# Optimization experiments

Measured on AMD Instinct MI355X. Metric: run time of the kernel, lower is better.

The kernel has to match this reference:

```python
import jax, jax.numpy as jnp
import numpy as np

GAMMA = 1.0

def setup_inputs() -> dict:
    key = jax.random.key(0)
    kx, ky = jax.random.split(key)
    x = jax.random.normal(kx, (8192, 256), dtype=jnp.float32)
    y = jax.random.normal(ky, (8192, 256), dtype=jnp.float32)
    return {"x": x, "y": y}

def reference(x, y):
    # RBF kernel K[i,j] = exp(-gamma * ||x_i - y_j||^2)
    # materializing the O(N*M*D) broadcast difference tensor.
    x2 = jnp.sum(x * x, axis=-1)            # [N]
    y2 = jnp.sum(y * y, axis=-1)            # [M]
    xy = jnp.einsum('nd,md->nm', x, y)      # [N, M] GEMM
    dist2 = x2[:, None] + y2[None, :] - 2.0 * xy
    dist2 = jnp.maximum(dist2, 0.0)         # guard tiny negative round-off
    return jnp.exp(-GAMMA * dist2)
```

## Files before the change

### kernel.cpp

```cpp
#include <hip/hip_runtime.h>


#define M_DIM 8192
#define K_DIM 256
#define BM 64
#define BN 64
#define TRS 68

typedef long frag8;
typedef __attribute__((ext_vector_type(4))) float float4v;

__global__ __launch_bounds__(256) void prep_kernel(
        const float* __restrict__ x, const float* __restrict__ y,
        unsigned char* __restrict__ xb, unsigned char* __restrict__ yb,
        float* __restrict__ x2, float* __restrict__ y2) {
    int row  = blockIdx.x * 4 + (threadIdx.x >> 6);
    int lane = threadIdx.x & 63;

    const float* src; unsigned char* dst; float* nrm; int r;
    if (row < M_DIM) { src = x; dst = xb; nrm = x2; r = row; }
    else             { src = y; dst = yb; nrm = y2; r = row - M_DIM; }

    const float4* s4 = (const float4*)(src + (size_t)r * K_DIM);
    float4 v = s4[lane];
    float ss = v.x * v.x + v.y * v.y + v.z * v.z + v.w * v.w;

    int packed = __builtin_amdgcn_cvt_pk_fp8_f32(v.x, v.y, 0, false);
    packed     = __builtin_amdgcn_cvt_pk_fp8_f32(v.z, v.w, packed, true);

    int u  = lane >> 2;
    int su = u ^ (r & 15);
    *(unsigned int*)(dst + (size_t)r * 256 + su * 16 + (lane & 3) * 4) =
        (unsigned int)packed;

    #pragma unroll
    for (int o = 32; o > 0; o >>= 1) ss += __shfl_down(ss, o);
    if (lane == 0) nrm[r] = ss;
}

__global__ __launch_bounds__(256, 4) void rbf_gemm(
        const unsigned char* __restrict__ xb, const unsigned char* __restrict__ yb,
        const float* __restrict__ x2, const float* __restrict__ y2,
        float* __restrict__ out) {
    __shared__ __align__(16) unsigned char smem[BM * 256 + BN * 256];
    unsigned char* As = smem;
    unsigned char* Bs = smem + BM * 256;
    float* T = (float*)smem;

    const int tid  = threadIdx.x;
    const int wid  = tid >> 6;
    const int lane = tid & 63;
    const int wm   = wid >> 1;
    const int wn   = wid & 1;

    const int bid = blockIdx.x;
    const int xcd = bid & 7;
    const int lin = bid >> 3;
    const int ty  = (xcd << 4) + (lin >> 7);
    const int tx  = lin & 127;
    const int m0  = ty * BM;
    const int n0  = tx * BN;

    #pragma unroll
    for (int i = 0; i < 4; ++i) {
        const int ch = wid * 4 + i;
        __builtin_amdgcn_global_load_lds(
            (__attribute__((address_space(1))) void*)
                (xb + (size_t)(m0 + ch * 4) * 256 + lane * 16),
            (__attribute__((address_space(3))) void*)&As[ch * 1024],
            16, 0, 0);
    }
    #pragma unroll
    for (int i = 0; i < 4; ++i) {
        const int ch = wid * 4 + i;
        __builtin_amdgcn_global_load_lds(
            (__attribute__((address_space(1))) void*)
                (yb + (size_t)(n0 + ch * 4) * 256 + lane * 16),
            (__attribute__((address_space(3))) void*)&Bs[ch * 1024],
            16, 0, 0);
    }

    const int q = lane >> 4;
    const int c = lane & 15;
    float x2v[2][4];
    float y2v[2];
    #pragma unroll
    for (int mt = 0; mt < 2; ++mt)
        #pragma unroll
        for (int v = 0; v < 4; ++v)
            x2v[mt][v] = x2[m0 + wm * 32 + mt * 16 + q * 4 + v];
    #pragma unroll
    for (int nt = 0; nt < 2; ++nt)
        y2v[nt] = y2[n0 + wn * 32 + nt * 16 + c];

    __syncthreads();

    const int fr = lane & 15;
    const int g  = lane >> 4;

    float4v acc[2][2] = {};

    #pragma unroll
    for (int ks = 0; ks < 8; ++ks) {
        const int off = (((2 * ks + (g >> 1)) ^ fr) << 4) + (g & 1) * 8;
        frag8 a[2], b[2];
        #pragma unroll
        for (int mt = 0; mt < 2; ++mt)
            a[mt] = *(const frag8*)&As[(wm * 32 + mt * 16 + fr) * 256 + off];
        #pragma unroll
        for (int nt = 0; nt < 2; ++nt)
            b[nt] = *(const frag8*)&Bs[(wn * 32 + nt * 16 + fr) * 256 + off];
        #pragma unroll
        for (int mt = 0; mt < 2; ++mt)
            #pragma unroll
            for (int nt = 0; nt < 2; ++nt)
                acc[mt][nt] = __builtin_amdgcn_mfma_f32_16x16x32_fp8_fp8(
                    a[mt], b[nt], acc[mt][nt], 0, 0, 0);
    }

    __syncthreads();

    #pragma unroll
    for (int mt = 0; mt < 2; ++mt) {
        #pragma unroll
        for (int nt = 0; nt < 2; ++nt) {
            #pragma unroll
            for (int v = 0; v < 4; ++v) {
                float d = x2v[mt][v] + y2v[nt] - 2.0f * acc[mt][nt][v];
                d = fmaxf(d, 0.0f);
                float r = 0.0f;
                if (__ballot(d < 105.0f) != 0ULL)
                    r = (d < 105.0f) ? __expf(-d) : 0.0f;
                T[(wm * 32 + mt * 16 + q * 4 + v) * TRS
                  + wn * 32 + nt * 16 + c] = r;
            }
        }
    }

    __syncthreads();

    const int rl = lane >> 4;
    const int cg = lane & 15;
    #pragma unroll
    for (int i = 0; i < 4; ++i) {
        const int r2 = wid * 16 + i * 4 + rl;
        float4v val = *(const float4v*)&T[r2 * TRS + cg * 4];
        *(float4v*)&out[(size_t)(m0 + r2) * M_DIM + n0 + cg * 4] = val;
    }
}

__global__ void rbf_naive(const float* __restrict__ x, const float* __restrict__ y,
                          float* __restrict__ out) {
    __shared__ float xs[16][17];
    __shared__ float ys[16][17];
    const int tx = threadIdx.x, ty = threadIdx.y;
    const int row = blockIdx.y * 16 + ty;
    const int col = blockIdx.x * 16 + tx;
    float acc = 0.0f;
    for (int k0 = 0; k0 < K_DIM; k0 += 16) {
        xs[ty][tx] = x[(size_t)row * K_DIM + k0 + tx];
        ys[ty][tx] = y[(size_t)(blockIdx.x * 16 + ty) * K_DIM + k0 + tx];
        __syncthreads();
        #pragma unroll
        for (int kk = 0; kk < 16; ++kk) {
            float d = xs[ty][kk] - ys[tx][kk];
            acc += d * d;
        }
        __syncthreads();
    }
    out[(size_t)row * M_DIM + col] = __expf(-acc);
}

extern "C" void kernel_launch(void* const* d_in, const int* in_sizes, int n_in,
                              void* d_out, int out_size, void* d_ws, size_t ws_size,
                              hipStream_t stream) {
    const float* x = (const float*)d_in[0];
    const float* y = (const float*)d_in[1];
    float* out = (float*)d_out;

    const size_t need = (size_t)2 * M_DIM * 256
                      + (size_t)2 * M_DIM * sizeof(float);
    if (ws_size >= need) {
        unsigned char* xb = (unsigned char*)d_ws;
        unsigned char* yb = xb + (size_t)M_DIM * 256;
        float* x2 = (float*)(yb + (size_t)M_DIM * 256);
        float* y2 = x2 + M_DIM;

        prep_kernel<<<dim3((2 * M_DIM) / 4), dim3(256), 0, stream>>>(x, y, xb, yb, x2, y2);
        rbf_gemm<<<dim3((M_DIM / BM) * (M_DIM / BN)), dim3(256), 0, stream>>>(xb, yb, x2, y2, out);
    } else {
        rbf_naive<<<dim3(M_DIM / 16, M_DIM / 16), dim3(16, 16), 0, stream>>>(x, y, out);
    }
}
```

Before: 280.8 us.

## Make GEMM blocks persistent over column tiles with double-buffered B loads

Each block now handles 8 consecutive column tiles for one row tile. The A tile stays resident in LDS, and the B tiles are double-buffered with async global-to-LDS loads so the next tile's load overlaps the current MFMA and epilogue. The LDS-staged transpose for coalesced float4 stores is removed, and results are written directly as scalar per-lane stores, which are less coalesced. LDS use grows and occupancy drops to 3 blocks per CU, with an eighth as many blocks launched.

```diff
diff --git a/kernel.cpp b/kernel.cpp
--- a/kernel.cpp
+++ b/kernel.cpp
@@ -5,7 +5,7 @@
 #define K_DIM 256
 #define BM 64
 #define BN 64
-#define TRS 68
+#define TPB 8
 
 typedef long frag8;
 typedef __attribute__((ext_vector_type(4))) float float4v;
@@ -38,14 +38,12 @@
     if (lane == 0) nrm[r] = ss;
 }
 
-__global__ __launch_bounds__(256, 4) void rbf_gemm(
+__global__ __launch_bounds__(256, 3) void rbf_gemm(
         const unsigned char* __restrict__ xb, const unsigned char* __restrict__ yb,
         const float* __restrict__ x2, const float* __restrict__ y2,
         float* __restrict__ out) {
-    __shared__ __align__(16) unsigned char smem[BM * 256 + BN * 256];
-    unsigned char* As = smem;
-    unsigned char* Bs = smem + BM * 256;
-    float* T = (float*)smem;
+    __shared__ __align__(16) unsigned char As[BM * 256];
+    __shared__ __align__(16) unsigned char Bs[2][BN * 256];
 
     const int tid  = threadIdx.x;
     const int wid  = tid >> 6;
@@ -56,10 +54,9 @@
     const int bid = blockIdx.x;
     const int xcd = bid & 7;
     const int lin = bid >> 3;
-    const int ty  = (xcd << 4) + (lin >> 7);
-    const int tx  = lin & 127;
+    const int ty  = (xcd << 4) + (lin >> 4);
+    const int tx0 = (lin & 15) * TPB;
     const int m0  = ty * BM;
-    const int n0  = tx * BN;
 
     #pragma unroll
     for (int i = 0; i < 4; ++i) {
@@ -75,77 +72,83 @@
         const int ch = wid * 4 + i;
         __builtin_amdgcn_global_load_lds(
             (__attribute__((address_space(1))) void*)
-                (yb + (size_t)(n0 + ch * 4) * 256 + lane * 16),
-            (__attribute__((address_space(3))) void*)&Bs[ch * 1024],
+                (yb + (size_t)(tx0 * BN + ch * 4) * 256 + lane * 16),
+            (__attribute__((address_space(3))) void*)&Bs[0][ch * 1024],
             16, 0, 0);
     }
 
-    const int q = lane >> 4;
-    const int c = lane & 15;
+    const int q  = lane >> 4;
+    const int c  = lane & 15;
+    const int fr = lane & 15;
+    const int g  = lane >> 4;
+
     float x2v[2][4];
-    float y2v[2];
     #pragma unroll
     for (int mt = 0; mt < 2; ++mt)
         #pragma unroll
         for (int v = 0; v < 4; ++v)
             x2v[mt][v] = x2[m0 + wm * 32 + mt * 16 + q * 4 + v];
-    #pragma unroll
-    for (int nt = 0; nt < 2; ++nt)
-        y2v[nt] = y2[n0 + wn * 32 + nt * 16 + c];
 
-    __syncthreads();
+    #pragma unroll 1
+    for (int t = 0; t < TPB; ++t) {
+        const int cur = t & 1;
+        const int n0  = (tx0 + t) * BN;
 
-    const int fr = lane & 15;
-    const int g  = lane >> 4;
+        __syncthreads();
 
-    float4v acc[2][2] = {};
+        if (t + 1 < TPB) {
+            #pragma unroll
+            for (int i = 0; i < 4; ++i) {
+                const int ch = wid * 4 + i;
+                __builtin_amdgcn_global_load_lds(
+                    (__attribute__((address_space(1))) void*)
+                        (yb + (size_t)((n0 + BN) + ch * 4) * 256 + lane * 16),
+                    (__attribute__((address_space(3))) void*)&Bs[cur ^ 1][ch * 1024],
+                    16, 0, 0);
+            }
+        }
 
-    #pragma unroll
-    for (int ks = 0; ks < 8; ++ks) {
-        const int off = (((2 * ks + (g >> 1)) ^ fr) << 4) + (g & 1) * 8;
-        frag8 a[2], b[2];
-        #pragma unroll
-        for (int mt = 0; mt < 2; ++mt)
-            a[mt] = *(const frag8*)&As[(wm * 32 + mt * 16 + fr) * 256 + off];
+        float y2v[2];
         #pragma unroll
         for (int nt = 0; nt < 2; ++nt)
-            b[nt] = *(const frag8*)&Bs[(wn * 32 + nt * 16 + fr) * 256 + off];
+            y2v[nt] = y2[n0 + wn * 32 + nt * 16 + c];
+
+        float4v acc[2][2] = {};
         #pragma unroll
-        for (int mt = 0; mt < 2; ++mt)
+        for (int ks = 0; ks < 8; ++ks) {
+            const int off = (((2 * ks + (g >> 1)) ^ fr) << 4) + (g & 1) * 8;
+            frag8 a[2], b[2];
+            #pragma unroll
+            for (int mt = 0; mt < 2; ++mt)
+                a[mt] = *(const frag8*)&As[(wm * 32 + mt * 16 + fr) * 256 + off];
             #pragma unroll
             for (int nt = 0; nt < 2; ++nt)
-                acc[mt][nt] = __builtin_amdgcn_mfma_f32_16x16x32_fp8_fp8(
-                    a[mt], b[nt], acc[mt][nt], 0, 0, 0);
-    }
+                b[nt] = *(const frag8*)&Bs[cur][(wn * 32 + nt * 16 + fr) * 256 + off];
+            #pragma unroll
+            for (int mt = 0; mt < 2; ++mt)
+                #pragma unroll
+                for (int nt = 0; nt < 2; ++nt)
+                    acc[mt][nt] = __builtin_amdgcn_mfma_f32_16x16x32_fp8_fp8(
+                        a[mt], b[nt], acc[mt][nt], 0, 0, 0);
+        }
 
-    __syncthreads();
-
-    #pragma unroll
-    for (int mt = 0; mt < 2; ++mt) {
         #pragma unroll
-        for (int nt = 0; nt < 2; ++nt) {
+        for (int mt = 0; mt < 2; ++mt) {
+            const int rowb = m0 + wm * 32 + mt * 16 + q * 4;
             #pragma unroll
-            for (int v = 0; v < 4; ++v) {
-                float d = x2v[mt][v] + y2v[nt] - 2.0f * acc[mt][nt][v];
-                d = fmaxf(d, 0.0f);
-                float r = 0.0f;
-                if (__ballot(d < 105.0f) != 0ULL)
-                    r = (d < 105.0f) ? __expf(-d) : 0.0f;
-                T[(wm * 32 + mt * 16 + q * 4 + v) * TRS
-                  + wn * 32 + nt * 16 + c] = r;
+            for (int nt = 0; nt < 2; ++nt) {
+                const int col = n0 + wn * 32 + nt * 16 + c;
+                #pragma unroll
+                for (int v = 0; v < 4; ++v) {
+                    float d = x2v[mt][v] + y2v[nt] - 2.0f * acc[mt][nt][v];
+                    d = fmaxf(d, 0.0f);
+                    float r = 0.0f;
+                    if (__ballot(d < 105.0f) != 0ULL)
+                        r = (d < 105.0f) ? __expf(-d) : 0.0f;
+                    out[(size_t)(rowb + v) * M_DIM + col] = r;
+                }
             }
         }
-    }
-
-    __syncthreads();
-
-    const int rl = lane >> 4;
-    const int cg = lane & 15;
-    #pragma unroll
-    for (int i = 0; i < 4; ++i) {
-        const int r2 = wid * 16 + i * 4 + rl;
-        float4v val = *(const float4v*)&T[r2 * TRS + cg * 4];
-        *(float4v*)&out[(size_t)(m0 + r2) * M_DIM + n0 + cg * 4] = val;
     }
 }
 
@@ -187,7 +190,8 @@
         float* y2 = x2 + M_DIM;
 
         prep_kernel<<<dim3((2 * M_DIM) / 4), dim3(256), 0, stream>>>(x, y, xb, yb, x2, y2);
-        rbf_gemm<<<dim3((M_DIM / BM) * (M_DIM / BN)), dim3(256), 0, stream>>>(xb, yb, x2, y2, out);
+        const int n_tiles = (M_DIM / BM) * (M_DIM / BN);
+        rbf_gemm<<<dim3(n_tiles / TPB), dim3(256), 0, stream>>>(xb, yb, x2, y2, out);
     } else {
         rbf_naive<<<dim3(M_DIM / 16, M_DIM / 16), dim3(16, 16), 0, stream>>>(x, y, out);
     }
```

Measured after the change: 284.6 us. No clear change (+1.4%).
